# Kernel tuning notes

Hardware: AMD Instinct MI355X
Metric: run time of the kernel (lower is better)

The kernel has to match this reference:

```python
import jax, jax.numpy as jnp
import numpy as np
from jax import lax

EPS = 1e-5  # flax BatchNorm default epsilon


def _conv(x, w, b, padding='SAME'):
    y = lax.conv_general_dilated(x, w, (1, 1), padding,
                                 dimension_numbers=('NHWC', 'HWIO', 'NHWC'))
    return y + b


def _maxpool(x, window, strides):
    return lax.reduce_window(x, -jnp.inf, lax.max,
                             (1,) + window + (1,), (1,) + strides + (1,), 'SAME')


def _bn_train(x, scale, bias):
    # training-mode BatchNorm: batch statistics over N,H,W
    m = x.mean(axis=(0, 1, 2))
    v = x.var(axis=(0, 1, 2))
    return (x - m) * lax.rsqrt(v + EPS) * scale + bias


def _lstm(x, wx, wh, b, carry, reverse):
    # x: (B, T, D); flax LSTMCell gate order i, f, g, o; bias lives on the
    # hidden dense in flax but is an equivalent single additive term here.
    xs = jnp.swapaxes(x @ wx + b, 0, 1)  # (T, B, 4H), input GEMM hoisted out of scan

    def step(ch, xt):
        c, h = ch
        g = xt + h @ wh
        i, f, gg, o = jnp.split(g, 4, axis=-1)
        c = jax.nn.sigmoid(f) * c + jax.nn.sigmoid(i) * jnp.tanh(gg)
        h = jax.nn.sigmoid(o) * jnp.tanh(c)
        return (c, h), h

    carry, ys = lax.scan(step, carry, xs, reverse=reverse)
    return carry, jnp.swapaxes(ys, 0, 1)  # (B, T, H)


def _forward(x, conv1_w, conv1_b, conv2_w, conv2_b, conv3_w, conv3_b, bn1_s, bn1_b,
             conv4_w, conv4_b, bn2_s, bn2_b, conv5_w, conv5_b, bn3_s, bn3_b,
             conv6_w, conv6_b, bn4_s, bn4_b, conv7_w, conv7_b, bn5_s, bn5_b,
             wq, bq, wk, bk, wv, bv,
             l1f_wx, l1f_wh, l1f_b, l1r_wx, l1r_wh, l1r_b,
             l2f_wx, l2f_wh, l2f_b, l2r_wx, l2r_wh, l2r_b, wo, bo):
    x = jax.nn.relu(_conv(x, conv1_w, conv1_b))
    x = _maxpool(x, (2, 2), (2, 2))
    x = jax.nn.relu(_conv(x, conv2_w, conv2_b))
    x = _maxpool(x, (2, 2), (2, 2))
    x = jax.nn.relu(_bn_train(_conv(x, conv3_w, conv3_b), bn1_s, bn1_b))
    x = jax.nn.relu(_bn_train(_conv(x, conv4_w, conv4_b), bn2_s, bn2_b))
    x = _maxpool(x, (2, 2), (1, 2))
    x = jax.nn.relu(_bn_train(_conv(x, conv5_w, conv5_b), bn3_s, bn3_b))
    x = jax.nn.relu(_bn_train(_conv(x, conv6_w, conv6_b), bn4_s, bn4_b))
    x = _maxpool(x, (2, 2), (1, 2))
    x = jax.nn.relu(_bn_train(_conv(x, conv7_w, conv7_b, padding='VALID'), bn5_s, bn5_b))
    B = x.shape[0]
    x = x.reshape(B, x.shape[1], -1)  # (B, T=H', W'*512); seq axis is height
    q = x @ wq + bq
    k = x @ wk + bk
    v = x @ wv + bv
    qk = jax.nn.softmax(jnp.einsum('btk,bsk->bts', q, k) / 32.0, axis=-1)
    x = jnp.einsum('btk,bts->bsk', v, qk)
    # stack 1: reverse LSTM deliberately starts from forward's FINAL carry (as in source)
    carry = (jnp.zeros((B, 256), x.dtype), jnp.zeros((B, 256), x.dtype))
    carry, y1 = _lstm(x, l1f_wx, l1f_wh, l1f_b, carry, reverse=False)
    carry, y2 = _lstm(x, l1r_wx, l1r_wh, l1r_b, carry, reverse=True)
    x1 = jnp.concatenate([y1, y2], axis=-1)
    # stack 2
    carry = (jnp.zeros((B, 512), x.dtype), jnp.zeros((B, 512), x.dtype))
    carry, y2b = _lstm(x1, l2f_wx, l2f_wh, l2f_b, carry, reverse=False)
    carry, y3 = _lstm(x1, l2r_wx, l2r_wh, l2r_b, carry, reverse=True)
    x = jnp.concatenate([y3, y2b], axis=-1)
    return x @ wo + bo


def setup_inputs() -> dict:
    key = jax.random.key(0)
    ks = iter(jax.random.split(key, 64))

    def cw(kh, kw, ci, co):
        return jax.random.normal(next(ks), (kh, kw, ci, co), jnp.float32) / np.float32(np.sqrt(kh * kw * ci))

    def dw(i, o):
        return jax.random.normal(next(ks), (i, o), jnp.float32) / np.float32(np.sqrt(i))

    z = lambda *s: jnp.zeros(s, jnp.float32)
    ones = lambda *s: jnp.ones(s, jnp.float32)
    class_nums = 1000
    d_in = 15 * 512  # W'=15 after conv stack, 512 channels
    inp = {
        'x': jax.random.normal(next(ks), (32, 64, 256, 3), jnp.float32),
        'conv1_w': cw(3, 3, 3, 64), 'conv1_b': z(64),
        'conv2_w': cw(3, 3, 64, 128), 'conv2_b': z(128),
        'conv3_w': cw(3, 3, 128, 256), 'conv3_b': z(256), 'bn1_s': ones(256), 'bn1_b': z(256),
        'conv4_w': cw(3, 3, 256, 256), 'conv4_b': z(256), 'bn2_s': ones(256), 'bn2_b': z(256),
        'conv5_w': cw(3, 3, 256, 512), 'conv5_b': z(512), 'bn3_s': ones(512), 'bn3_b': z(512),
        'conv6_w': cw(3, 3, 512, 512), 'conv6_b': z(512), 'bn4_s': ones(512), 'bn4_b': z(512),
        'conv7_w': cw(2, 2, 512, 512), 'conv7_b': z(512), 'bn5_s': ones(512), 'bn5_b': z(512),
        'wq': dw(d_in, 512), 'bq': z(512),
        'wk': dw(d_in, 512), 'bk': z(512),
        'wv': dw(d_in, 512), 'bv': z(512),
        'l1f_wx': dw(512, 4 * 256), 'l1f_wh': dw(256, 4 * 256), 'l1f_b': z(4 * 256),
        'l1r_wx': dw(512, 4 * 256), 'l1r_wh': dw(256, 4 * 256), 'l1r_b': z(4 * 256),
        'l2f_wx': dw(512, 4 * 512), 'l2f_wh': dw(512, 4 * 512), 'l2f_b': z(4 * 512),
        'l2r_wx': dw(512, 4 * 512), 'l2r_wh': dw(512, 4 * 512), 'l2r_b': z(4 * 512),
        'wo': dw(1024, class_nums), 'bo': z(class_nums),
    }
    return inp


def reference(x, conv1_w, conv1_b, conv2_w, conv2_b, conv3_w, conv3_b, bn1_s, bn1_b,
              conv4_w, conv4_b, bn2_s, bn2_b, conv5_w, conv5_b, bn3_s, bn3_b,
              conv6_w, conv6_b, bn4_s, bn4_b, conv7_w, conv7_b, bn5_s, bn5_b,
              wq, bq, wk, bk, wv, bv,
              l1f_wx, l1f_wh, l1f_b, l1r_wx, l1r_wh, l1r_b,
              l2f_wx, l2f_wh, l2f_b, l2r_wx, l2r_wh, l2r_b, wo, bo):
    return _forward(x, conv1_w, conv1_b, conv2_w, conv2_b, conv3_w, conv3_b, bn1_s, bn1_b,
                    conv4_w, conv4_b, bn2_s, bn2_b, conv5_w, conv5_b, bn3_s, bn3_b,
                    conv6_w, conv6_b, bn4_s, bn4_b, conv7_w, conv7_b, bn5_s, bn5_b,
                    wq, bq, wk, bk, wv, bv,
                    l1f_wx, l1f_wh, l1f_b, l1r_wx, l1r_wh, l1r_b,
                    l2f_wx, l2f_wh, l2f_b, l2r_wx, l2r_wh, l2r_b, wo, bo)
```

## Files before the change

kernel.cpp:

```cpp
#include <hip/hip_runtime.h>
#include <math.h>

#define DIV_UP(a,b) (((a)+(b)-1)/(b))

typedef _Float16 half_t;
typedef _Float16 half8 __attribute__((ext_vector_type(8)));
typedef float f32x4 __attribute__((ext_vector_type(4)));

#define FLAG_RELU   1
#define FLAG_OUTF32 2
#define FLAG_SPLITK 4
#define FLAG_ATOMIC 8
#define FLAG_BNSUMS 16

#define GLDS16(src, dst) \
  __builtin_amdgcn_global_load_lds((const __attribute__((address_space(1))) void*)(src), \
                                   (__attribute__((address_space(3))) void*)(dst), 16, 0, 0)

__device__ __forceinline__ float fsig_(float x){ return 1.0f/(1.0f+__expf(-x)); }
__device__ __forceinline__ float ftanh_(float x){
  float ax = fabsf(x);
  float e = __expf(-2.0f*ax);
  float t = (1.0f - e)/(1.0f + e);
  return copysignf(t, x);
}

struct TpAll {
  const float* src[14];
  half_t* dst[14];
  int K[14];
  int N[14];
  int prefix[15];
};

__global__ __launch_bounds__(256) void transpose_cvt_all_kernel(TpAll a)
{
  __shared__ float tile[32][33];
  int bid = blockIdx.x;
  int z = 0;
  while (bid >= a.prefix[z+1]) ++z;
  int local = bid - a.prefix[z];
  const float* w = a.src[z];
  half_t* wT = a.dst[z];
  int K = a.K[z], N = a.N[z];
  int tilesX = (N + 31) >> 5;
  int nt = (local % tilesX) * 32;
  int kt = (local / tilesX) * 32;
  int tx = threadIdx.x & 31, ty = threadIdx.x >> 5;
  #pragma unroll
  for (int r = 0; r < 4; ++r) {
    int k = kt + ty + r*8, n = nt + tx;
    tile[ty + r*8][tx] = (k < K && n < N) ? w[(long)k*N + n] : 0.f;
  }
  __syncthreads();
  #pragma unroll
  for (int r = 0; r < 4; ++r) {
    int n = nt + ty + r*8, k = kt + tx;
    if (n < N && k < K) wT[(long)n*K + k] = (half_t)tile[tx][ty + r*8];
  }
}

__global__ __launch_bounds__(256) void conv1_kernel(
    const float* __restrict__ x, const float* __restrict__ w,
    const float* __restrict__ bias, half_t* __restrict__ out)
{
  __shared__ float xs[3][258*3];
  int nb = blockIdx.x;
  int n = nb >> 6, ho = nb & 63;
  int tid = threadIdx.x;
  int co = tid & 63;
  float wreg[27];
  #pragma unroll
  for (int k = 0; k < 27; ++k) wreg[k] = w[k*64 + co];
  float bco = bias[co];
  for (int i = tid; i < 3*258*3; i += 256) {
    int row = i / (258*3); int rem = i % (258*3);
    int col = rem / 3;     int ci  = rem % 3;
    int ih = ho - 1 + row; int iw = col - 1;
    float v = 0.f;
    if (ih >= 0 && ih < 64 && iw >= 0 && iw < 256)
      v = x[(((long)n*64 + ih)*256 + iw)*3 + ci];
    xs[row][col*3 + ci] = v;
  }
  __syncthreads();
  int wave = tid >> 6;
  for (int p = 0; p < 64; ++p) {
    int wo = wave*64 + p;
    float acc = bco;
    #pragma unroll
    for (int kh = 0; kh < 3; ++kh)
      #pragma unroll
      for (int kw = 0; kw < 3; ++kw)
        #pragma unroll
        for (int ci = 0; ci < 3; ++ci)
          acc = fmaf(xs[kh][(wo+kw)*3 + ci], wreg[(kh*3+kw)*3 + ci], acc);
    acc = fmaxf(acc, 0.f);
    out[(((long)n*64 + ho)*256 + wo)*64 + co] = (half_t)acc;
  }
}

struct GOut { const half_t* wT; const float* bias; void* out; };

__global__ __launch_bounds__(256) void mfma_conv_kernel(
    const half_t* __restrict__ x, GOut g0, GOut g1, GOut g2,
    const half_t* __restrict__ zbuf, float* __restrict__ bns,
    int N,int H,int W,int Ci,int Ho,int Wo,int Co,
    int KH,int KW,int padH,int padW,
    int M,int K,int flags,int splitS)
{
  GOut g;
  int ciBeg = 0, ciEnd = Ci;
  if (flags & FLAG_SPLITK) {
    g = g0;
    int span = Ci / splitS;
    ciBeg = blockIdx.z * span;
    ciEnd = ciBeg + span;
  } else {
    g = (blockIdx.z == 0) ? g0 : (blockIdx.z == 1 ? g1 : g2);
  }
  const half_t* __restrict__ wT = g.wT;
  __shared__ half_t As[128*64];
  __shared__ half_t Bs[128*64];
  int tid = threadIdx.x;
  int m0 = blockIdx.y*128, n0 = blockIdx.x*128;
  int wave = tid >> 6, lane = tid & 63;
  int l15 = lane & 15, quad = lane >> 4;
  int x7 = lane & 7;
  int wm = (wave & 1) * 64, wn = (wave >> 1) * 64;

  int rSub = tid >> 3;
  int colHalf = (((tid & 7) ^ (rSub & 7))) * 8;

  int ho_[4], wo_[4], ni_[4]; bool av_[4];
  #pragma unroll
  for (int i = 0; i < 4; ++i) {
    int m = m0 + i*32 + rSub;
    av_[i] = m < M;
    int mm = av_[i] ? m : 0;
    wo_[i] = mm % Wo; int t2 = mm / Wo;
    ho_[i] = t2 % Ho; ni_[i] = t2 / Ho;
  }
  const half_t* bBase[4];
  #pragma unroll
  for (int i = 0; i < 4; ++i) {
    int n = n0 + i*32 + rSub;
    bBase[i] = (n < Co) ? (wT + (long)n*K + colHalf) : nullptr;
  }

  int pch0 = ((quad)     ^ x7) * 8;
  int pch1 = ((4 + quad) ^ x7) * 8;

  f32x4 acc[4][4];
  #pragma unroll
  for (int i = 0; i < 4; ++i)
    #pragma unroll
    for (int j = 0; j < 4; ++j)
      acc[i][j] = (f32x4){0.f, 0.f, 0.f, 0.f};

  int kg = ciBeg;
  for (int kh = 0; kh < KH; ++kh) {
    for (int kw = 0; kw < KW; ++kw) {
      long aOff[4]; bool aval[4];
      #pragma unroll
      for (int i = 0; i < 4; ++i) {
        int ih = ho_[i] - padH + kh, iw = wo_[i] - padW + kw;
        bool ok = av_[i] && ih >= 0 && ih < H && iw >= 0 && iw < W;
        aval[i] = ok;
        aOff[i] = ok ? ((((long)ni_[i]*H + ih)*W + iw)*(long)Ci + colHalf) : 0;
      }
      for (int ci = ciBeg; ci < ciEnd; ci += 64, kg += 64) {
        #pragma unroll
        for (int i = 0; i < 4; ++i) {
          const half_t* sa = aval[i] ? (x + aOff[i] + ci) : zbuf;
          GLDS16(sa, As + i*2048 + wave*512);
          const half_t* sb = bBase[i] ? (bBase[i] + kg) : zbuf;
          GLDS16(sb, Bs + i*2048 + wave*512);
        }
        __syncthreads();
        {
          half8 af[4], bf[4];
          #pragma unroll
          for (int i = 0; i < 4; ++i)
            af[i] = *reinterpret_cast<half8*>(&As[(wm + i*16 + l15)*64 + pch0]);
          #pragma unroll
          for (int j = 0; j < 4; ++j)
            bf[j] = *reinterpret_cast<half8*>(&Bs[(wn + j*16 + l15)*64 + pch0]);
          #pragma unroll
          for (int i = 0; i < 4; ++i)
            #pragma unroll
            for (int j = 0; j < 4; ++j)
              acc[i][j] = __builtin_amdgcn_mfma_f32_16x16x32_f16(af[i], bf[j], acc[i][j], 0, 0, 0);
        }
        {
          half8 af[4], bf[4];
          #pragma unroll
          for (int i = 0; i < 4; ++i)
            af[i] = *reinterpret_cast<half8*>(&As[(wm + i*16 + l15)*64 + pch1]);
          #pragma unroll
          for (int j = 0; j < 4; ++j)
            bf[j] = *reinterpret_cast<half8*>(&Bs[(wn + j*16 + l15)*64 + pch1]);
          #pragma unroll
          for (int i = 0; i < 4; ++i)
            #pragma unroll
            for (int j = 0; j < 4; ++j)
              acc[i][j] = __builtin_amdgcn_mfma_f32_16x16x32_f16(af[i], bf[j], acc[i][j], 0, 0, 0);
        }
        __syncthreads();
      }
    }
  }

  if (flags & FLAG_BNSUMS) {
    float* red = (float*)As;
    #pragma unroll
    for (int j = 0; j < 4; ++j) {
      int n = n0 + wn + j*16 + l15;
      float bv = g.bias[n];
      float s = 0.f, q = 0.f;
      #pragma unroll
      for (int i = 0; i < 4; ++i)
        #pragma unroll
        for (int r = 0; r < 4; ++r) {
          int m = m0 + wm + i*16 + quad*4 + r;
          if (m < M) { float v = acc[i][j][r] + bv; s += v; q += v*v; }
        }
      int idx = ((((wave*4 + quad)*16 + l15)*4) + j)*2;
      red[idx] = s; red[idx+1] = q;
    }
    __syncthreads();
    if (tid < 128) {
      int hi = tid >> 6;
      int jj = (tid >> 4) & 3, ll = tid & 15;
      float s = 0.f, q = 0.f;
      #pragma unroll
      for (int w2 = 0; w2 < 2; ++w2)
        #pragma unroll
        for (int qd = 0; qd < 4; ++qd) {
          int idx = (((((hi*2 + w2)*4 + qd)*16 + ll)*4) + jj)*2;
          s += red[idx]; q += red[idx+1];
        }
      int n = n0 + tid;
      atomicAdd(&bns[n], s);
      atomicAdd(&bns[Co + n], q);
    }
  }

  #pragma unroll
  for (int i = 0; i < 4; ++i) {
    #pragma unroll
    for (int r = 0; r < 4; ++r) {
      int m = m0 + wm + i*16 + quad*4 + r;
      if (m >= M) continue;
      #pragma unroll
      for (int j = 0; j < 4; ++j) {
        int n = n0 + wn + j*16 + l15;
        if (n >= Co) continue;
        if (flags & FLAG_ATOMIC) {
          atomicAdd(&((float*)g.out)[(long)m*Co + n], acc[i][j][r]);
        } else {
          float v = acc[i][j][r] + g.bias[n];
          if (flags & FLAG_RELU) v = fmaxf(v, 0.f);
          if (flags & FLAG_OUTF32) ((float*)g.out)[(long)m*Co + n] = v;
          else ((half_t*)g.out)[(long)m*Co + n] = (half_t)v;
        }
      }
    }
  }
}

__global__ __launch_bounds__(256) void maxpool8_kernel(
    const half_t* __restrict__ x, half_t* __restrict__ out,
    int N,int H,int W,int C,int Ho,int Wo,int sH,int sW)
{
  int C8 = C >> 3;
  long idx = (long)blockIdx.x*256 + threadIdx.x;
  long total8 = (long)N*Ho*Wo*C8;
  if (idx >= total8) return;
  int cb = (int)(idx % C8);
  long pix = idx / C8;
  int wo = (int)(pix % Wo); long t2 = pix / Wo;
  int ho = (int)(t2 % Ho); int n = (int)(t2 / Ho);
  int c = cb * 8;
  float m[8];
  #pragma unroll
  for (int e = 0; e < 8; ++e) m[e] = -INFINITY;
  for (int i = 0; i < 2; ++i) {
    int ih = ho*sH + i;
    if (ih >= H) continue;
    for (int j = 0; j < 2; ++j) {
      int iw = wo*sW + j;
      if (iw >= W) continue;
      half8 v = *reinterpret_cast<const half8*>(x + (((long)n*H + ih)*W + iw)*C + c);
      #pragma unroll
      for (int e = 0; e < 8; ++e) m[e] = fmaxf(m[e], (float)v[e]);
    }
  }
  half8 o;
  #pragma unroll
  for (int e = 0; e < 8; ++e) o[e] = (half_t)m[e];
  *reinterpret_cast<half8*>(out + idx*8) = o;
}

__global__ __launch_bounds__(256) void bn_apply_relu8_kernel(
    half_t* __restrict__ x, const float* __restrict__ sums,
    const float* __restrict__ scale, const float* __restrict__ bias,
    long total8, int C, float invN)
{
  long idx = (long)blockIdx.x*256 + threadIdx.x;
  if (idx >= total8) return;
  int c = (int)((idx*8) % C);
  half8 v = *reinterpret_cast<half8*>(x + idx*8);
  half8 o;
  #pragma unroll
  for (int e = 0; e < 8; ++e) {
    float mean = sums[c+e] * invN;
    float var  = sums[C + c+e] * invN - mean*mean;
    float rstd = rsqrtf(var + 1e-5f);
    float y = ((float)v[e] - mean) * rstd * scale[c+e] + bias[c+e];
    o[e] = (half_t)fmaxf(y, 0.0f);
  }
  *reinterpret_cast<half8*>(x + idx*8) = o;
}

__global__ __launch_bounds__(256) void bn_pool8_kernel(
    const half_t* __restrict__ x, half_t* __restrict__ out,
    const float* __restrict__ sums, const float* __restrict__ scale,
    const float* __restrict__ bias,
    int N,int H,int W,int C,int Ho,int Wo,int sH,int sW, float invN)
{
  int C8 = C >> 3;
  long idx = (long)blockIdx.x*256 + threadIdx.x;
  long total8 = (long)N*Ho*Wo*C8;
  if (idx >= total8) return;
  int cb = (int)(idx % C8);
  long pix = idx / C8;
  int wo = (int)(pix % Wo); long t2 = pix / Wo;
  int ho = (int)(t2 % Ho); int n = (int)(t2 / Ho);
  int c = cb * 8;
  float mean[8], rs[8], bb[8];
  #pragma unroll
  for (int e = 0; e < 8; ++e) {
    mean[e] = sums[c+e] * invN;
    float var = sums[C + c+e] * invN - mean[e]*mean[e];
    rs[e] = rsqrtf(var + 1e-5f) * scale[c+e];
    bb[e] = bias[c+e];
  }
  float m[8];
  #pragma unroll
  for (int e = 0; e < 8; ++e) m[e] = -INFINITY;
  for (int i = 0; i < 2; ++i) {
    int ih = ho*sH + i;
    if (ih >= H) continue;
    for (int j = 0; j < 2; ++j) {
      int iw = wo*sW + j;
      if (iw >= W) continue;
      half8 v = *reinterpret_cast<const half8*>(x + (((long)n*H + ih)*W + iw)*C + c);
      #pragma unroll
      for (int e = 0; e < 8; ++e) {
        float y = fmaxf(((float)v[e] - mean[e]) * rs[e] + bb[e], 0.f);
        m[e] = fmaxf(m[e], y);
      }
    }
  }
  half8 o;
  #pragma unroll
  for (int e = 0; e < 8; ++e) o[e] = (half_t)m[e];
  *reinterpret_cast<half8*>(out + idx*8) = o;
}

__global__ __launch_bounds__(256) void bias_fill_kernel(
    float* __restrict__ out, const float* __restrict__ b0,
    const float* __restrict__ b1, const float* __restrict__ b2, int total)
{
  int idx = blockIdx.x*256 + threadIdx.x;
  if (idx >= total) return;
  int n = idx % 1536;
  float v = (n < 512) ? b0[n] : (n < 1024 ? b1[n-512] : b2[n-1024]);
  out[idx] = v;
}

__global__ __launch_bounds__(256) void attention_kernel(
    const float* __restrict__ qkv, half_t* __restrict__ out,
    int T, int D, int ld)
{
  int b = blockIdx.x;
  int tid = threadIdx.x;
  __shared__ float P[15][16];
  if (tid < T*T) {
    int t = tid / T, s = tid % T;
    const float* qp = qkv + ((long)b*T + t)*ld;
    const float* kp = qkv + ((long)b*T + s)*ld + 512;
    float acc = 0.f;
    for (int d = 0; d < D; d += 4) {
      float4 qv = *reinterpret_cast<const float4*>(qp + d);
      float4 kv = *reinterpret_cast<const float4*>(kp + d);
      acc += qv.x*kv.x + qv.y*kv.y + qv.z*kv.z + qv.w*kv.w;
    }
    P[t][s] = acc * (1.0f/32.0f);
  }
  __syncthreads();
  if (tid < T) {
    float mx = -INFINITY;
    for (int s = 0; s < T; ++s) mx = fmaxf(mx, P[tid][s]);
    float sum = 0.f;
    for (int s = 0; s < T; ++s) { float e = expf(P[tid][s] - mx); P[tid][s] = e; sum += e; }
    float inv = 1.0f / sum;
    for (int s = 0; s < T; ++s) P[tid][s] *= inv;
  }
  __syncthreads();
  for (int idx = tid; idx < T*D; idx += 256) {
    int s = idx / D, kk2 = idx % D;
    float acc = 0.f;
    #pragma unroll
    for (int t = 0; t < 15; ++t)
      acc += qkv[((long)b*T + t)*ld + 1024 + kk2] * P[t][s];
    out[((long)b*T + s)*D + kk2] = (half_t)acc;
  }
}

#define MAXK 512
#define HSROW (MAXK + 8)

template<int N64, int HLOG>
__device__ __forceinline__ void stage_h(
    const unsigned long long* __restrict__ src, half_t (*hs)[HSROW], int tid)
{
  unsigned long long tmp[N64];
  #pragma unroll
  for (int u = 0; u < N64; ++u)
    tmp[u] = __hip_atomic_load(src + tid + u*256, __ATOMIC_RELAXED, __HIP_MEMORY_SCOPE_AGENT);
  #pragma unroll
  for (int u = 0; u < N64; ++u) {
    int idx = tid + u*256;
    int row = idx >> (HLOG - 2);
    int col = (idx & ((1 << (HLOG - 2)) - 1)) * 4;
    *reinterpret_cast<unsigned long long*>(&hs[row][col]) = tmp[u];
  }
}

template<int H>
__global__ __launch_bounds__(256, 1) void lstm_persistent_kernel(
    const float* __restrict__ preF, const float* __restrict__ preR,
    const float* __restrict__ whF, const float* __restrict__ whR,
    half_t* __restrict__ hbuf, half_t* __restrict__ y,
    int* __restrict__ flags, int nblk,
    int ystride, int yoffF, int yoffR)
{
  constexpr int KI = H / 32;
  constexpr int H4 = 4 * H;
  __shared__ half_t hs[32][HSROW];
  __shared__ float gates[32][133];
  int tid = threadIdx.x;
  int jb0 = blockIdx.x * 32;
  int lane = tid & 63, wave = tid >> 6;
  int l15 = lane & 15, quad = lane >> 4;
  int bb = tid >> 3;
  int jj0 = (tid & 7) * 4;

  float cst[4] = {0.f, 0.f, 0.f, 0.f};
  half8 wreg[2][KI];

  auto loadw = [&](const float* __restrict__ wh) {
    #pragma unroll
    for (int f = 0; f < 2; ++f) {
      int col = wave*H + jb0 + f*16 + l15;
      #pragma unroll
      for (int i = 0; i < KI; ++i) {
        half8 v;
        #pragma unroll
        for (int e = 0; e < 8; ++e)
          v[e] = (half_t)wh[(long)(i*32 + quad*8 + e)*H4 + col];
        wreg[f][i] = v;
      }
    }
  };

  loadw(whF);
  const float* pre = preF;
  int yoff = yoffF;

  for (int s = 0; s < 30; ++s) {
    if (s == 15) {
      loadw(whR);
      pre = preR; yoff = yoffR;
    }
    int t = (s < 15) ? s : 29 - s;

    float pv[16];
    {
      const float* pp = pre + (long)(bb*15 + t)*H4 + jb0 + jj0;
      #pragma unroll
      for (int g = 0; g < 4; ++g) {
        f32x4 v = *reinterpret_cast<const f32x4*>(pp + g*H);
        pv[g*4+0] = v[0]; pv[g*4+1] = v[1]; pv[g*4+2] = v[2]; pv[g*4+3] = v[3];
      }
    }

    const unsigned long long* hsrc =
        (const unsigned long long*)(hbuf + (long)(s & 1) * 32 * H);
    if constexpr (H == 512) stage_h<16, 9>(hsrc, hs, tid);
    else                    stage_h<8, 8>(hsrc, hs, tid);
    __syncthreads();

    f32x4 acc00 = {0.f,0.f,0.f,0.f}, acc10 = {0.f,0.f,0.f,0.f};
    f32x4 acc01 = {0.f,0.f,0.f,0.f}, acc11 = {0.f,0.f,0.f,0.f};
    #pragma unroll
    for (int i = 0; i < KI; ++i) {
      half8 a0 = *reinterpret_cast<half8*>(&hs[l15][i*32 + quad*8]);
      half8 a1 = *reinterpret_cast<half8*>(&hs[16 + l15][i*32 + quad*8]);
      acc00 = __builtin_amdgcn_mfma_f32_16x16x32_f16(a0, wreg[0][i], acc00, 0, 0, 0);
      acc10 = __builtin_amdgcn_mfma_f32_16x16x32_f16(a1, wreg[0][i], acc10, 0, 0, 0);
      acc01 = __builtin_amdgcn_mfma_f32_16x16x32_f16(a0, wreg[1][i], acc01, 0, 0, 0);
      acc11 = __builtin_amdgcn_mfma_f32_16x16x32_f16(a1, wreg[1][i], acc11, 0, 0, 0);
    }
    #pragma unroll
    for (int r = 0; r < 4; ++r) {
      gates[quad*4 + r][wave*32 + l15]           = acc00[r];
      gates[16 + quad*4 + r][wave*32 + l15]      = acc10[r];
      gates[quad*4 + r][wave*32 + 16 + l15]      = acc01[r];
      gates[16 + quad*4 + r][wave*32 + 16 + l15] = acc11[r];
    }
    __syncthreads();

    unsigned long long hpack;
    {
      half_t hn[4];
      #pragma unroll
      for (int p = 0; p < 4; ++p) {
        int j = jj0 + p;
        float gi = pv[p]      + gates[bb][j];
        float gf = pv[4 + p]  + gates[bb][32 + j];
        float gg = pv[8 + p]  + gates[bb][64 + j];
        float go = pv[12 + p] + gates[bb][96 + j];
        gi = fsig_(gi); gf = fsig_(gf); gg = ftanh_(gg); go = fsig_(go);
        float cn = gf * cst[p] + gi * gg;
        cst[p] = cn;
        hn[p] = (half_t)(go * ftanh_(cn));
      }
      hpack = *reinterpret_cast<unsigned long long*>(hn);
      half_t* hdst = hbuf + (long)((s + 1) & 1) * 32 * H;
      __hip_atomic_store((unsigned long long*)(hdst + (long)bb*H + jb0 + jj0), hpack,
                         __ATOMIC_RELAXED, __HIP_MEMORY_SCOPE_AGENT);
    }

    if (s < 29) {
      __syncthreads();
      if (tid == 0)
        __hip_atomic_store(&flags[blockIdx.x], s + 1,
                           __ATOMIC_RELAXED, __HIP_MEMORY_SCOPE_AGENT);
      *reinterpret_cast<unsigned long long*>(
          &y[(long)(bb*15 + t)*ystride + yoff + jb0 + jj0]) = hpack;
      if (tid < 64) {
        int target = s + 1;
        for (;;) {
          int vv = (tid < nblk)
            ? __hip_atomic_load(&flags[tid], __ATOMIC_RELAXED, __HIP_MEMORY_SCOPE_AGENT)
            : target;
          if (__all(vv >= target)) break;
        }
      }
      __syncthreads();
    } else {
      *reinterpret_cast<unsigned long long*>(
          &y[(long)(bb*15 + t)*ystride + yoff + jb0 + jj0]) = hpack;
    }
  }
}

extern "C" void kernel_launch(void* const* d_in, const int* in_sizes, int n_in,
                              void* d_out, int out_size, void* d_ws, size_t ws_size,
                              hipStream_t stream)
{
  const float* x       = (const float*)d_in[0];
  const float* c1w     = (const float*)d_in[1];  const float* c1b = (const float*)d_in[2];
  const float* c2w     = (const float*)d_in[3];  const float* c2b = (const float*)d_in[4];
  const float* c3w     = (const float*)d_in[5];  const float* c3b = (const float*)d_in[6];
  const float* bn1s    = (const float*)d_in[7];  const float* bn1b = (const float*)d_in[8];
  const float* c4w     = (const float*)d_in[9];  const float* c4b = (const float*)d_in[10];
  const float* bn2s    = (const float*)d_in[11]; const float* bn2b = (const float*)d_in[12];
  const float* c5w     = (const float*)d_in[13]; const float* c5b = (const float*)d_in[14];
  const float* bn3s    = (const float*)d_in[15]; const float* bn3b = (const float*)d_in[16];
  const float* c6w     = (const float*)d_in[17]; const float* c6b = (const float*)d_in[18];
  const float* bn4s    = (const float*)d_in[19]; const float* bn4b = (const float*)d_in[20];
  const float* c7w     = (const float*)d_in[21]; const float* c7b = (const float*)d_in[22];
  const float* bn5s    = (const float*)d_in[23]; const float* bn5b = (const float*)d_in[24];
  const float* wq      = (const float*)d_in[25]; const float* bq = (const float*)d_in[26];
  const float* wk      = (const float*)d_in[27]; const float* bk = (const float*)d_in[28];
  const float* wv      = (const float*)d_in[29]; const float* bv = (const float*)d_in[30];
  const float* l1f_wx  = (const float*)d_in[31]; const float* l1f_wh = (const float*)d_in[32]; const float* l1f_b = (const float*)d_in[33];
  const float* l1r_wx  = (const float*)d_in[34]; const float* l1r_wh = (const float*)d_in[35]; const float* l1r_b = (const float*)d_in[36];
  const float* l2f_wx  = (const float*)d_in[37]; const float* l2f_wh = (const float*)d_in[38]; const float* l2f_b = (const float*)d_in[39];
  const float* l2r_wx  = (const float*)d_in[40]; const float* l2r_wh = (const float*)d_in[41]; const float* l2r_b = (const float*)d_in[42];
  const float* wo      = (const float*)d_in[43]; const float* bo = (const float*)d_in[44];
  float* outp = (float*)d_out;

  char* base = (char*)d_ws;
  half_t* actA = (half_t*)base;
  half_t* actB = (half_t*)(base + 67108864);
  half_t* wtA  = (half_t*)(base + 100663296);
  float*  f32a = (float*)(base + 143687680);
  half_t* h16a = (half_t*)(base + 158736384);

  half_t* wt2  = wtA;
  half_t* wt3  = wtA + 73728;
  half_t* wt4  = wtA + 368640;
  half_t* wt5  = wtA + 958464;
  half_t* wt6  = wtA + 2138112;
  half_t* wt7  = wtA + 4497408;
  half_t* wtq  = wtA + 5545984;
  half_t* wtk  = wtA + 9478144;
  half_t* wtv  = wtA + 13410304;
  half_t* wt1f = wtA + 17342464;
  half_t* wt1r = wtA + 17866752;
  half_t* wt2f = wtA + 18391040;
  half_t* wt2r = wtA + 19439616;
  half_t* wto  = wtA + 20488192;

  float* qkvbuf = f32a;
  float* pre1f = f32a + 737280;
  float* pre1r = f32a + 1228800;
  float* pre2f = f32a + 1720320;
  float* pre2r = f32a + 2703360;

  half_t* ao  = h16a;
  half_t* x1  = h16a + 245760;
  half_t* x2  = h16a + 491520;
  half_t* hb1 = h16a + 983040;
  half_t* hb2 = hb1 + 16384;
  int*    flags1 = (int*)(hb2 + 32768);
  int*    flags2 = flags1 + 512;
  half_t* zbuf   = (half_t*)(flags2 + 512);
  float*  bnz    = (float*)(zbuf + 32);

  auto convm = [&](const half_t* in, const half_t* wt, const float* b, void* out,
                   int N,int H,int W,int Ci,int Ho,int Wo,int Co,
                   int KH,int KW,int pH,int pW,int flags, float* bns){
    int M = N*Ho*Wo, K = KH*KW*Ci;
    dim3 grid(DIV_UP(Co,128), DIV_UP(M,128), 1);
    GOut g{wt, b, out};
    mfma_conv_kernel<<<grid,256,0,stream>>>(in,g,g,g,zbuf,bns,N,H,W,Ci,Ho,Wo,Co,
                                            KH,KW,pH,pW,M,K,flags,1);
  };
  auto gemm3 = [&](const half_t* A, GOut g0, GOut g1, GOut g2, int nz,
                   int M, int Nn, int K, int flags, int splitS){
    dim3 grid(DIV_UP(Nn,128), DIV_UP(M,128), nz);
    mfma_conv_kernel<<<grid,256,0,stream>>>(A,g0,g1,g2,zbuf,bnz,M,1,1,K,1,1,Nn,
                                            1,1,0,0,M,K,flags,splitS);
  };
  auto pool = [&](const half_t* in, half_t* out, int N,int H,int W,int C,
                  int Ho,int Wo,int sH,int sW){
    long total8 = (long)N*Ho*Wo*(C/8);
    maxpool8_kernel<<<(int)DIV_UP(total8,256),256,0,stream>>>(in,out,N,H,W,C,Ho,Wo,sH,sW);
  };
  auto bnApply = [&](half_t* buf, long nPix, int C, const float* s, const float* b,
                     float* sums){
    long total8 = nPix * C / 8;
    bn_apply_relu8_kernel<<<(int)DIV_UP(total8,256),256,0,stream>>>(buf, sums, s, b, total8, C, 1.0f/(float)nPix);
  };
  auto bnPool = [&](const half_t* in, half_t* out, int N,int H,int W,int C,
                    int Ho,int Wo,int sH,int sW, long nPix,
                    const float* s, const float* b, float* sums){
    long total8 = (long)N*Ho*Wo*(C/8);
    bn_pool8_kernel<<<(int)DIV_UP(total8,256),256,0,stream>>>(
        in,out,sums,s,b,N,H,W,C,Ho,Wo,sH,sW,1.0f/(float)nPix);
  };

  hipMemsetAsync(hb1, 0, 143424, stream);

  {
    TpAll tp;
    const float* srcs[14] = {c2w,c3w,c4w,c5w,c6w,c7w,wq,wk,wv,l1f_wx,l1r_wx,l2f_wx,l2r_wx,wo};
    half_t* dsts[14] = {wt2,wt3,wt4,wt5,wt6,wt7,wtq,wtk,wtv,wt1f,wt1r,wt2f,wt2r,wto};
    int Ks[14] = {576,1152,2304,2304,4608,2048,7680,7680,7680,512,512,512,512,1024};
    int Ns[14] = {128,256,256,512,512,512,512,512,512,1024,1024,2048,2048,1000};
    int acc = 0;
    for (int i = 0; i < 14; ++i) {
      tp.src[i] = srcs[i]; tp.dst[i] = dsts[i]; tp.K[i] = Ks[i]; tp.N[i] = Ns[i];
      tp.prefix[i] = acc;
      acc += DIV_UP(Ks[i],32) * DIV_UP(Ns[i],32);
    }
    tp.prefix[14] = acc;
    transpose_cvt_all_kernel<<<acc,256,0,stream>>>(tp);
  }

  conv1_kernel<<<2048,256,0,stream>>>(x, c1w, c1b, actA);
  pool(actA, actB, 32,64,256,64,  32,128, 2,2);
  convm(actB, wt2, c2b, actA, 32,32,128,64,  32,128,128, 3,3,1,1, FLAG_RELU, bnz);
  pool(actA, actB, 32,32,128,128, 16,64, 2,2);
  convm(actB, wt3, c3b, actA, 32,16,64,128,  16,64,256,  3,3,1,1, FLAG_BNSUMS, bnz);
  bnApply(actA, 32768, 256, bn1s, bn1b, bnz);
  convm(actA, wt4, c4b, actB, 32,16,64,256,  16,64,256,  3,3,1,1, FLAG_BNSUMS, bnz + 2048);
  bnPool(actB, actA, 32,16,64,256, 16,32, 1,2, 32768, bn2s, bn2b, bnz + 2048);
  convm(actA, wt5, c5b, actB, 32,16,32,256,  16,32,512,  3,3,1,1, FLAG_BNSUMS, bnz + 4096);
  bnApply(actB, 16384, 512, bn3s, bn3b, bnz + 4096);
  convm(actB, wt6, c6b, actA, 32,16,32,512,  16,32,512,  3,3,1,1, FLAG_BNSUMS, bnz + 6144);
  bnPool(actA, actB, 32,16,32,512, 16,16, 1,2, 16384, bn4s, bn4b, bnz + 6144);
  convm(actB, wt7, c7b, actA, 32,16,16,512,  15,15,512,  2,2,0,0, FLAG_BNSUMS, bnz + 8192);
  bnApply(actA, 7200, 512, bn5s, bn5b, bnz + 8192);

  bias_fill_kernel<<<DIV_UP(480*1536,256),256,0,stream>>>(qkvbuf, bq, bk, bv, 480*1536);
  gemm3(actA, GOut{wtq, nullptr, qkvbuf}, GOut{wtq, nullptr, qkvbuf},
        GOut{wtq, nullptr, qkvbuf}, 4, 480, 1536, 7680, FLAG_SPLITK|FLAG_ATOMIC, 4);
  attention_kernel<<<32,256,0,stream>>>(qkvbuf, ao, 15, 512, 1536);

  gemm3(ao, GOut{wt1f, l1f_b, pre1f}, GOut{wt1r, l1r_b, pre1r},
        GOut{wt1r, l1r_b, pre1r}, 2, 480, 1024, 512, FLAG_OUTF32, 1);
  lstm_persistent_kernel<256><<<8,256,0,stream>>>(
      pre1f, pre1r, l1f_wh, l1r_wh, hb1, x1, flags1, 8, 512, 0, 256);

  gemm3(x1, GOut{wt2f, l2f_b, pre2f}, GOut{wt2r, l2r_b, pre2r},
        GOut{wt2r, l2r_b, pre2r}, 2, 480, 2048, 512, FLAG_OUTF32, 1);
  lstm_persistent_kernel<512><<<16,256,0,stream>>>(
      pre2f, pre2r, l2f_wh, l2r_wh, hb2, x2, flags2, 16, 1024, 512, 0);

  gemm3(x2, GOut{wto, bo, outp}, GOut{wto, bo, outp}, GOut{wto, bo, outp}, 1,
        480, 1000, 1024, FLAG_OUTF32, 1);
}
```

Before: 1.172 ms.

## Pre-transpose LSTM recurrent weights to fp16 and prefetch next-step pre-gates

Adds the four LSTM recurrent weight matrices to the batched transpose/convert kernel, so each lane loads contiguous half8 vectors instead of strided scalar fp32 loads with per-element conversion. The load at the direction switch and at start becomes cheap. The next step's pre-activation gate values are also loaded while the block spins on the inter-block barrier, hiding that global load latency. In exchange the up-front transpose kernel gets more tiles and more scratch memory is used at fixed offsets.

```diff
diff --git a/kernel.cpp b/kernel.cpp
--- a/kernel.cpp
+++ b/kernel.cpp
@@ -25,12 +25,13 @@
   return copysignf(t, x);
 }
 
+#define NTP 18
 struct TpAll {
-  const float* src[14];
-  half_t* dst[14];
-  int K[14];
-  int N[14];
-  int prefix[15];
+  const float* src[NTP];
+  half_t* dst[NTP];
+  int K[NTP];
+  int N[NTP];
+  int prefix[NTP+1];
 };
 
 __global__ __launch_bounds__(256) void transpose_cvt_all_kernel(TpAll a)
@@ -441,13 +442,12 @@
 template<int H>
 __global__ __launch_bounds__(256, 1) void lstm_persistent_kernel(
     const float* __restrict__ preF, const float* __restrict__ preR,
-    const float* __restrict__ whF, const float* __restrict__ whR,
+    const half_t* __restrict__ whTF, const half_t* __restrict__ whTR,
     half_t* __restrict__ hbuf, half_t* __restrict__ y,
     int* __restrict__ flags, int nblk,
     int ystride, int yoffF, int yoffR)
 {
   constexpr int KI = H / 32;
-  constexpr int H4 = 4 * H;
   __shared__ half_t hs[32][HSROW];
   __shared__ float gates[32][133];
   int tid = threadIdx.x;
@@ -456,45 +456,40 @@
   int l15 = lane & 15, quad = lane >> 4;
   int bb = tid >> 3;
   int jj0 = (tid & 7) * 4;
+  constexpr int H4 = 4 * H;
 
   float cst[4] = {0.f, 0.f, 0.f, 0.f};
   half8 wreg[2][KI];
 
-  auto loadw = [&](const float* __restrict__ wh) {
+  auto loadw = [&](const half_t* __restrict__ whT) {
     #pragma unroll
     for (int f = 0; f < 2; ++f) {
-      int col = wave*H + jb0 + f*16 + l15;
-      #pragma unroll
-      for (int i = 0; i < KI; ++i) {
-        half8 v;
-        #pragma unroll
-        for (int e = 0; e < 8; ++e)
-          v[e] = (half_t)wh[(long)(i*32 + quad*8 + e)*H4 + col];
-        wreg[f][i] = v;
-      }
+      const half_t* wp = whT + (long)(wave*H + jb0 + f*16 + l15)*H + quad*8;
+      #pragma unroll
+      for (int i = 0; i < KI; ++i)
+        wreg[f][i] = *reinterpret_cast<const half8*>(wp + i*32);
     }
   };
 
-  loadw(whF);
-  const float* pre = preF;
-  int yoff = yoffF;
+  auto loadpv = [&](int s, float (&pv)[16]) {
+    const float* pr = (s < 15) ? preF : preR;
+    int t = (s < 15) ? s : 29 - s;
+    const float* pp = pr + (long)(bb*15 + t)*H4 + jb0 + jj0;
+    #pragma unroll
+    for (int g = 0; g < 4; ++g) {
+      f32x4 v = *reinterpret_cast<const f32x4*>(pp + g*H);
+      pv[g*4+0] = v[0]; pv[g*4+1] = v[1]; pv[g*4+2] = v[2]; pv[g*4+3] = v[3];
+    }
+  };
+
+  loadw(whTF);
+  float pv[16];
+  loadpv(0, pv);
 
   for (int s = 0; s < 30; ++s) {
-    if (s == 15) {
-      loadw(whR);
-      pre = preR; yoff = yoffR;
-    }
+    if (s == 15) loadw(whTR);
     int t = (s < 15) ? s : 29 - s;
-
-    float pv[16];
-    {
-      const float* pp = pre + (long)(bb*15 + t)*H4 + jb0 + jj0;
-      #pragma unroll
-      for (int g = 0; g < 4; ++g) {
-        f32x4 v = *reinterpret_cast<const f32x4*>(pp + g*H);
-        pv[g*4+0] = v[0]; pv[g*4+1] = v[1]; pv[g*4+2] = v[2]; pv[g*4+3] = v[3];
-      }
-    }
+    int yoff = (s < 15) ? yoffF : yoffR;
 
     const unsigned long long* hsrc =
         (const unsigned long long*)(hbuf + (long)(s & 1) * 32 * H);
@@ -550,6 +545,7 @@
                            __ATOMIC_RELAXED, __HIP_MEMORY_SCOPE_AGENT);
       *reinterpret_cast<unsigned long long*>(
           &y[(long)(bb*15 + t)*ystride + yoff + jb0 + jj0]) = hpack;
+      loadpv(s + 1, pv);
       if (tid < 64) {
         int target = s + 1;
         for (;;) {
@@ -631,6 +627,11 @@
   int*    flags2 = flags1 + 512;
   half_t* zbuf   = (half_t*)(flags2 + 512);
   float*  bnz    = (float*)(zbuf + 32);
+
+  half_t* whT1f = (half_t*)(base + 160849920);
+  half_t* whT1r = (half_t*)(base + 161374208);
+  half_t* whT2f = (half_t*)(base + 161898496);
+  half_t* whT2r = (half_t*)(base + 163995648);
 
   auto convm = [&](const half_t* in, const half_t* wt, const float* b, void* out,
                    int N,int H,int W,int Ci,int Ho,int Wo,int Co,
@@ -669,17 +670,21 @@
 
   {
     TpAll tp;
-    const float* srcs[14] = {c2w,c3w,c4w,c5w,c6w,c7w,wq,wk,wv,l1f_wx,l1r_wx,l2f_wx,l2r_wx,wo};
-    half_t* dsts[14] = {wt2,wt3,wt4,wt5,wt6,wt7,wtq,wtk,wtv,wt1f,wt1r,wt2f,wt2r,wto};
-    int Ks[14] = {576,1152,2304,2304,4608,2048,7680,7680,7680,512,512,512,512,1024};
-    int Ns[14] = {128,256,256,512,512,512,512,512,512,1024,1024,2048,2048,1000};
+    const float* srcs[NTP] = {c2w,c3w,c4w,c5w,c6w,c7w,wq,wk,wv,l1f_wx,l1r_wx,l2f_wx,l2r_wx,wo,
+                              l1f_wh,l1r_wh,l2f_wh,l2r_wh};
+    half_t* dsts[NTP] = {wt2,wt3,wt4,wt5,wt6,wt7,wtq,wtk,wtv,wt1f,wt1r,wt2f,wt2r,wto,
+                         whT1f,whT1r,whT2f,whT2r};
+    int Ks[NTP] = {576,1152,2304,2304,4608,2048,7680,7680,7680,512,512,512,512,1024,
+                   256,256,512,512};
+    int Ns[NTP] = {128,256,256,512,512,512,512,512,512,1024,1024,2048,2048,1000,
+                   1024,1024,2048,2048};
     int acc = 0;
-    for (int i = 0; i < 14; ++i) {
+    for (int i = 0; i < NTP; ++i) {
       tp.src[i] = srcs[i]; tp.dst[i] = dsts[i]; tp.K[i] = Ks[i]; tp.N[i] = Ns[i];
       tp.prefix[i] = acc;
       acc += DIV_UP(Ks[i],32) * DIV_UP(Ns[i],32);
     }
-    tp.prefix[14] = acc;
+    tp.prefix[NTP] = acc;
     transpose_cvt_all_kernel<<<acc,256,0,stream>>>(tp);
   }
 
@@ -706,12 +711,12 @@
   gemm3(ao, GOut{wt1f, l1f_b, pre1f}, GOut{wt1r, l1r_b, pre1r},
         GOut{wt1r, l1r_b, pre1r}, 2, 480, 1024, 512, FLAG_OUTF32, 1);
   lstm_persistent_kernel<256><<<8,256,0,stream>>>(
-      pre1f, pre1r, l1f_wh, l1r_wh, hb1, x1, flags1, 8, 512, 0, 256);
+      pre1f, pre1r, whT1f, whT1r, hb1, x1, flags1, 8, 512, 0, 256);
 
   gemm3(x1, GOut{wt2f, l2f_b, pre2f}, GOut{wt2r, l2r_b, pre2r},
         GOut{wt2r, l2r_b, pre2r}, 2, 480, 2048, 512, FLAG_OUTF32, 1);
   lstm_persistent_kernel<512><<<16,256,0,stream>>>(
-      pre2f, pre2r, l2f_wh, l2r_wh, hb2, x2, flags2, 16, 1024, 512, 0);
+      pre2f, pre2r, whT2f, whT2r, hb2, x2, flags2, 16, 1024, 512, 0);
 
   gemm3(x2, GOut{wto, bo, outp}, GOut{wto, bo, outp}, GOut{wto, bo, outp}, 1,
         480, 1000, 1024, FLAG_OUTF32, 1);
```

Measured after the change: 1.059 ms. 9.6% less time.
